# Performance work log

Measured on AMD Instinct MI355X. Metric: run time of the kernel, lower is better.

Reference implementation:

```python
import jax, jax.numpy as jnp
import numpy as np

B = 512            # graphs in batch
N = 246            # ROIs per graph per node type (Brainnetome atlas)
D = 256            # node feature dim (in_channels)
DEG = 32           # edges per node per edge type
RATIO = 0.8
K = int(np.ceil(RATIO * N))   # 197 nodes kept per graph (PyG topk uses ceil)
NT = B * N                    # total nodes per node type
E = B * N * DEG               # total edges per edge type
SLOPE = 0.2                   # HANConv leaky_relu negative slope


def _seg_softmax(logits, seg, num_segments):
    # numerically stable softmax over edges grouped by destination node
    m = jax.ops.segment_max(logits, seg, num_segments=num_segments)
    m = jnp.where(jnp.isfinite(m), m, 0.0)
    e = jnp.exp(logits - m[seg])
    s = jax.ops.segment_sum(e, seg, num_segments=num_segments)
    return e / (s[seg] + 1e-16)


def _edge_type_out(h_src, h_dst, ei, a_src, a_dst, n_dst):
    # one HANConv metapath: GAT-style attention + sum-aggregate + relu
    row, col = ei[0], ei[1]
    logit = jax.nn.leaky_relu((h_src * a_src).sum(-1)[row] + (h_dst * a_dst).sum(-1)[col], SLOPE)
    alpha = _seg_softmax(logit, col, n_dst)
    out = jax.ops.segment_sum(h_src[row] * alpha[:, None], col, num_segments=n_dst)
    return jax.nn.relu(out)


def _group(o1, o2, k_w, k_b, q):
    # HANConv semantic attention over the 2 metapaths hitting a node type
    stk = jnp.stack([o1, o2])                    # [2, NT, 1]
    t = jnp.tanh(stk @ k_w + k_b).mean(axis=1)   # [2, 1]
    w = jax.nn.softmax((q * t).sum(-1))          # [2]
    return (w[:, None, None] * stk).sum(0)       # [NT, 1]


def _han_scores(x_bold, x_dti, pw_b, pb_b, pw_d, pb_d, att, k_w, k_b, q, ei_bb, ei_bd, ei_db, ei_dd):
    h_b = x_bold @ pw_b + pb_b   # [NT, 1]
    h_d = x_dti @ pw_d + pb_d
    o_bb = _edge_type_out(h_b, h_b, ei_bb, att[0, 0], att[0, 1], NT)  # dst bold
    o_bd = _edge_type_out(h_b, h_d, ei_bd, att[1, 0], att[1, 1], NT)  # dst dti
    o_db = _edge_type_out(h_d, h_b, ei_db, att[2, 0], att[2, 1], NT)  # dst bold
    o_dd = _edge_type_out(h_d, h_d, ei_dd, att[3, 0], att[3, 1], NT)  # dst dti
    s_bold = _group(o_bb, o_db, k_w, k_b, q)[:, 0]
    s_dti = _group(o_bd, o_dd, k_w, k_b, q)[:, 0]
    return s_bold, s_dti


def _topk(score):
    # per-graph top-K (all graphs have exactly N nodes -> static K)
    _, idx = jax.lax.top_k(score.reshape(B, N), K)
    return (idx + (jnp.arange(B, dtype=idx.dtype) * N)[:, None]).reshape(-1)


def _mask_of(perm, num_nodes):
    return jnp.full((num_nodes,), -1, dtype=jnp.int32).at[perm].set(
        jnp.arange(perm.shape[0], dtype=jnp.int32))


def _filter(ei, mask_row, mask_col):
    # jit-compatible variant of filter_adj: keep full edge length, mark
    # dropped edges with -1 and return the validity mask (no compaction).
    r, c = mask_row[ei[0]], mask_col[ei[1]]
    valid = (r >= 0) & (c >= 0)
    return jnp.stack([jnp.where(valid, r, -1), jnp.where(valid, c, -1)]), valid


def setup_inputs() -> dict:
    key = jax.random.key(0)
    ks = jax.random.split(key, 12)

    def edges(k):
        k1, k2 = jax.random.split(k)
        base = jnp.repeat(jnp.arange(B, dtype=jnp.int32) * N, N * DEG)
        row = base + jax.random.randint(k1, (E,), 0, N, dtype=jnp.int32)
        col = base + jax.random.randint(k2, (E,), 0, N, dtype=jnp.int32)
        return jnp.stack([row, col])

    batch = jnp.repeat(jnp.arange(B, dtype=jnp.int32), N)
    return {
        "x_bold": jax.random.normal(ks[0], (NT, D), jnp.float32),
        "x_dti": jax.random.normal(ks[1], (NT, D), jnp.float32),
        "proj_w_bold": jax.random.normal(ks[2], (D, 1), jnp.float32) / np.float32(np.sqrt(D)),
        "proj_b_bold": jnp.zeros((1,), jnp.float32),
        "proj_w_dti": jax.random.normal(ks[3], (D, 1), jnp.float32) / np.float32(np.sqrt(D)),
        "proj_b_dti": jnp.zeros((1,), jnp.float32),
        "att": jax.random.normal(ks[4], (4, 2, 1), jnp.float32),
        "k_lin_w": jax.random.normal(ks[5], (1, 1), jnp.float32),
        "k_lin_b": jnp.zeros((1,), jnp.float32),
        "q": jax.random.normal(ks[6], (1,), jnp.float32),
        "ei_bb": edges(ks[7]),
        "ei_bd": edges(ks[8]),
        "ei_db": edges(ks[9]),
        "ei_dd": edges(ks[10]),
        "batch_bold": batch,
        "batch_dti": batch,
    }


def reference(x_bold, x_dti, proj_w_bold, proj_b_bold, proj_w_dti, proj_b_dti,
              att, k_lin_w, k_lin_b, q, ei_bb, ei_bd, ei_db, ei_dd,
              batch_bold, batch_dti):
    s_bold, s_dti = _han_scores(x_bold, x_dti, proj_w_bold, proj_b_bold,
                                proj_w_dti, proj_b_dti, att, k_lin_w, k_lin_b, q,
                                ei_bb, ei_bd, ei_db, ei_dd)
    perm_b = _topk(s_bold)
    perm_d = _topk(s_dti)
    xb = x_bold[perm_b] * jnp.tanh(s_bold[perm_b])[:, None]
    xd = x_dti[perm_d] * jnp.tanh(s_dti[perm_d])[:, None]
    mb = _mask_of(perm_b, NT)
    md = _mask_of(perm_d, NT)
    bb_f, v_bb = _filter(ei_bb, mb, mb)   # filter_adj_single on bold-bold
    dd_f, v_dd = _filter(ei_dd, md, md)   # filter_adj_single on dti-dti
    bd_f, v_bd = _filter(ei_bd, mb, md)   # filter_adj_multi mode=1
    db_f, v_db = _filter(ei_db, md, mb)   # filter_adj_multi mode=2
    return (xb, xd, bb_f, v_bb, bd_f, v_bd, db_f, v_db, dd_f, v_dd,
            batch_bold[perm_b], batch_dti[perm_d], perm_b, perm_d, s_bold, s_dti)
```

## Files before the change

kernel.cpp:

```cpp
#include <hip/hip_runtime.h>
#include <cmath>

#define BB   512
#define NN   246
#define DD   256
#define DEGC 32
#define KK   197
#define NTOT (BB*NN)
#define EE   (BB*NN*DEGC)
#define EPG  (NN*DEGC)
#define EPG4 (EPG/4)
#define BKK  (BB*KK)

#define O_XB     0LL
#define O_XD     25821184LL
#define O_E0     51642368LL
#define STRIDE3E 12091392LL
#define O_BATCHB 100007936LL
#define O_BATCHD 100108800LL
#define O_PERMB  100209664LL
#define O_PERMD  100310528LL
#define O_SB     100411392LL
#define O_SD     100537344LL

__global__ __launch_bounds__(256) void proj_kernel(
    const float* __restrict__ xb, const float* __restrict__ xd,
    const float* __restrict__ wb, const float* __restrict__ bbp,
    const float* __restrict__ wd, const float* __restrict__ bdp,
    float* __restrict__ hb, float* __restrict__ hd,
    double* __restrict__ sums) {
    if (blockIdx.x == 0 && threadIdx.x < 4) sums[threadIdx.x] = 0.0;
    int wid  = (blockIdx.x * 256 + threadIdx.x) >> 6;
    int lane = threadIdx.x & 63;
    if (wid >= 2 * NTOT) return;
    const float* x; const float* w; const float* bp; float* h; int node;
    if (wid < NTOT) { x = xb; w = wb; bp = bbp; h = hb; node = wid; }
    else            { x = xd; w = wd; bp = bdp; h = hd; node = wid - NTOT; }
    float4 xv = ((const float4*)(x + (long long)node * DD))[lane];
    float4 wv = ((const float4*)w)[lane];
    double acc = (double)xv.x * wv.x + (double)xv.y * wv.y +
                 (double)xv.z * wv.z + (double)xv.w * wv.w;
#pragma unroll
    for (int m = 32; m; m >>= 1) acc += __shfl_xor(acc, m, 64);
    if (lane == 0) h[node] = __fadd_rn((float)acc, bp[0]);
}

__global__ __launch_bounds__(512) void att_kernel(
    const int* __restrict__ ei_bb, const int* __restrict__ ei_bd,
    const int* __restrict__ ei_db, const int* __restrict__ ei_dd,
    const float* __restrict__ hb, const float* __restrict__ hd,
    const float* __restrict__ att, float* __restrict__ o) {
    __shared__ float hs_sh[NN];
    __shared__ float hd_sh[NN];
    __shared__ float s_sh[NN];
    __shared__ float num_sh[NN];

    int bid = blockIdx.x;
    int t   = bid >> 9;
    int g   = bid & 511;
    const int* ei = (t == 0) ? ei_bb : (t == 1) ? ei_bd : (t == 2) ? ei_db : ei_dd;
    const float* hs  = (t >= 2) ? hd : hb;
    const float* hdt = (t & 1)  ? hd : hb;
    float a_src = att[2 * t], a_dst = att[2 * t + 1];
    int base = g * NN;
    int tid  = threadIdx.x;

    if (tid < NN) {
        hs_sh[tid]  = hs[base + tid];
        hd_sh[tid]  = hdt[base + tid];
        s_sh[tid]   = 1e-16f;
        num_sh[tid] = 0.f;
    }
    __syncthreads();

    const int4* rows = (const int4*)(ei + g * EPG);
    const int4* cols = (const int4*)(ei + EE + g * EPG);

    for (int q = tid; q < EPG4; q += 512) {
        int4 r4 = rows[q], c4 = cols[q];
#pragma unroll
        for (int j = 0; j < 4; ++j) {
            int r = ((const int*)&r4)[j] - base;
            int c = ((const int*)&c4)[j] - base;
            float hr = hs_sh[r];
            float l  = __fadd_rn(__fmul_rn(a_src, hr), __fmul_rn(a_dst, hd_sh[c]));
            l = (l >= 0.f) ? l : __fmul_rn(0.2f, l);
            float e = expf(l);
            atomicAdd(&s_sh[c], e);
            atomicAdd(&num_sh[c], __fmul_rn(hr, e));
        }
    }
    __syncthreads();

    if (tid < NN) {
        float v = num_sh[tid] / s_sh[tid];
        o[(long long)t * NTOT + base + tid] = (v > 0.f) ? v : 0.f;
    }
}

__global__ __launch_bounds__(256) void grp_reduce_kernel(
    const float* __restrict__ o, const float* __restrict__ kwp,
    const float* __restrict__ kbp, double* __restrict__ sums) {
    int i = blockIdx.x * 256 + threadIdx.x;
    int t = blockIdx.x / 492;
    float kw = kwp[0], kb = kbp[0];
    float v = tanhf(__fadd_rn(__fmul_rn(o[i], kw), kb));
    double acc = (double)v;
#pragma unroll
    for (int m = 32; m; m >>= 1) acc += __shfl_xor(acc, m, 64);
    __shared__ double part[4];
    int lane = threadIdx.x & 63, wv = threadIdx.x >> 6;
    if (lane == 0) part[wv] = acc;
    __syncthreads();
    if (threadIdx.x == 0) {
        double tot = ((part[0] + part[1]) + part[2]) + part[3];
        atomicAdd(&sums[t], tot);
    }
}

__global__ void grp_w_kernel(const double* __restrict__ sums,
                             const float* __restrict__ qp,
                             float* __restrict__ wscal) {
    if (threadIdx.x == 0 && blockIdx.x == 0) {
        float q = qp[0];
        float tv[4];
#pragma unroll
        for (int i = 0; i < 4; ++i) tv[i] = (float)(sums[i] / (double)NTOT);
        {
            float l0 = __fmul_rn(q, tv[0]), l1 = __fmul_rn(q, tv[2]);
            float mx = fmaxf(l0, l1);
            float e0 = expf(l0 - mx), e1 = expf(l1 - mx);
            float se = __fadd_rn(e0, e1);
            wscal[0] = e0 / se; wscal[1] = e1 / se;
        }
        {
            float l0 = __fmul_rn(q, tv[1]), l1 = __fmul_rn(q, tv[3]);
            float mx = fmaxf(l0, l1);
            float e0 = expf(l0 - mx), e1 = expf(l1 - mx);
            float se = __fadd_rn(e0, e1);
            wscal[2] = e0 / se; wscal[3] = e1 / se;
        }
    }
}

__global__ __launch_bounds__(256) void score_kernel(
    const float* __restrict__ o, const float* __restrict__ wscal,
    float* __restrict__ sb, float* __restrict__ sd,
    float* __restrict__ osb, float* __restrict__ osd) {
    int i = blockIdx.x * 256 + threadIdx.x;
    float w0 = wscal[0], w1 = wscal[1], w2 = wscal[2], w3 = wscal[3];
    float vb = __fadd_rn(__fmul_rn(w0, o[i]),          __fmul_rn(w1, o[2LL * NTOT + i]));
    float vd = __fadd_rn(__fmul_rn(w2, o[NTOT + i]),   __fmul_rn(w3, o[3LL * NTOT + i]));
    sb[i] = vb; sd[i] = vd; osb[i] = vb; osd[i] = vd;
}

__global__ __launch_bounds__(256) void topk_kernel(
    const float* __restrict__ sb, const float* __restrict__ sd,
    const int* __restrict__ batch_b, const int* __restrict__ batch_d,
    int* __restrict__ mask_b, int* __restrict__ mask_d,
    int* __restrict__ perm_b, int* __restrict__ perm_d,
    float* __restrict__ out) {
    __shared__ float v[256];
    __shared__ int   ix[256];
    int g = blockIdx.x & 511, which = blockIdx.x >> 9, tid = threadIdx.x;
    const float* s     = which ? sd : sb;
    const int*   batch = which ? batch_d : batch_b;
    int* mask  = which ? mask_d : mask_b;
    int* permi = which ? perm_d : perm_b;
    float* operm  = out + (which ? O_PERMD : O_PERMB);
    float* obatch = out + (which ? O_BATCHD : O_BATCHB);
    v[tid]  = (tid < NN) ? s[g * NN + tid] : -INFINITY;
    ix[tid] = tid;
    __syncthreads();
    for (int k2 = 2; k2 <= 256; k2 <<= 1) {
        for (int j = k2 >> 1; j > 0; j >>= 1) {
            int p = tid ^ j;
            if (p > tid) {
                float va = v[tid], vb2 = v[p];
                int   ia = ix[tid], ib = ix[p];
                bool before = (va > vb2) || (va == vb2 && ia < ib);
                bool up = ((tid & k2) == 0);
                if (up ? !before : before) {
                    v[tid] = vb2; v[p] = va; ix[tid] = ib; ix[p] = ia;
                }
            }
            __syncthreads();
        }
    }
    if (tid < NN) {
        int node  = ix[tid];
        int gnode = g * NN + node;
        if (tid < KK) {
            int gp = g * KK + tid;
            permi[gp]  = gnode;
            operm[gp]  = (float)gnode;
            obatch[gp] = (float)batch[gnode];
            mask[gnode] = gp;
        } else {
            mask[gnode] = -1;
        }
    }
}

__global__ __launch_bounds__(256) void gather_kernel(
    const float* __restrict__ xb, const float* __restrict__ xd,
    const int* __restrict__ perm_b, const int* __restrict__ perm_d,
    const float* __restrict__ sb, const float* __restrict__ sd,
    float* __restrict__ out) {
    int wid  = (blockIdx.x * 256 + threadIdx.x) >> 6;
    int lane = threadIdx.x & 63;
    if (wid >= 2 * BKK) return;
    int which = wid >= BKK;
    int j = which ? wid - BKK : wid;
    const float* x    = which ? xd : xb;
    const int*   perm = which ? perm_d : perm_b;
    const float* s    = which ? sd : sb;
    long long obase   = which ? O_XD : O_XB;
    int p = perm[j];
    float scale = tanhf(s[p]);
    float4 vv = ((const float4*)(x + (long long)p * DD))[lane];
    float4 r  = make_float4(vv.x * scale, vv.y * scale, vv.z * scale, vv.w * scale);
    ((float4*)(out + obase + (long long)j * DD))[lane] = r;
}

__global__ __launch_bounds__(256) void filter_kernel(
    const int* __restrict__ ei_bb, const int* __restrict__ ei_bd,
    const int* __restrict__ ei_db, const int* __restrict__ ei_dd,
    const int* __restrict__ mask_b, const int* __restrict__ mask_d,
    float* __restrict__ out) {
    const int QE = EE / 4;
    int tid = blockIdx.x * 256 + threadIdx.x;
    if (tid >= 4 * QE) return;
    int t = tid / QE;
    int q = tid - t * QE;
    const int* ei = (t == 0) ? ei_bb : (t == 1) ? ei_bd : (t == 2) ? ei_db : ei_dd;
    const int* mr = (t >= 2) ? mask_d : mask_b;
    const int* mc = (t & 1)  ? mask_d : mask_b;
    int4 r4 = ((const int4*)ei)[q];
    int4 c4 = ((const int4*)(ei + EE))[q];
    float4 orow, ocol, oval;
#pragma unroll
    for (int j = 0; j < 4; ++j) {
        int r = mr[((const int*)&r4)[j]];
        int c = mc[((const int*)&c4)[j]];
        bool val = (r >= 0) && (c >= 0);
        ((float*)&orow)[j] = val ? (float)r : -1.f;
        ((float*)&ocol)[j] = val ? (float)c : -1.f;
        ((float*)&oval)[j] = val ? 1.f : 0.f;
    }
    float* base = out + O_E0 + (long long)t * STRIDE3E;
    ((float4*)base)[q]              = orow;
    ((float4*)(base + EE))[q]       = ocol;
    ((float4*)(base + 2LL * EE))[q] = oval;
}

extern "C" void kernel_launch(void* const* d_in, const int* in_sizes, int n_in,
                              void* d_out, int out_size, void* d_ws, size_t ws_size,
                              hipStream_t stream) {
    const float* x_bold = (const float*)d_in[0];
    const float* x_dti  = (const float*)d_in[1];
    const float* pw_b   = (const float*)d_in[2];
    const float* pb_b   = (const float*)d_in[3];
    const float* pw_d   = (const float*)d_in[4];
    const float* pb_d   = (const float*)d_in[5];
    const float* att    = (const float*)d_in[6];
    const float* k_w    = (const float*)d_in[7];
    const float* k_b    = (const float*)d_in[8];
    const float* qv     = (const float*)d_in[9];
    const int* ei_bb    = (const int*)d_in[10];
    const int* ei_bd    = (const int*)d_in[11];
    const int* ei_db    = (const int*)d_in[12];
    const int* ei_dd    = (const int*)d_in[13];
    const int* batch_b  = (const int*)d_in[14];
    const int* batch_d  = (const int*)d_in[15];
    float* out = (float*)d_out;

    char* w = (char*)d_ws;
    double* sums  = (double*)w;
    float*  wscal = (float*)(w + 32);
    float*  hb    = (float*)(w + 48);
    float*  hd    = hb + NTOT;
    float*  obuf  = hd + NTOT;
    float*  sb    = obuf + 4LL * NTOT;
    float*  sd    = sb + NTOT;
    int* mask_b   = (int*)(sd + NTOT);
    int* mask_d   = mask_b + NTOT;
    int* perm_b   = mask_d + NTOT;
    int* perm_d   = perm_b + BKK;

    proj_kernel<<<2 * NTOT / 4, 256, 0, stream>>>(x_bold, x_dti, pw_b, pb_b,
                                                  pw_d, pb_d, hb, hd, sums);
    att_kernel<<<4 * BB, 512, 0, stream>>>(ei_bb, ei_bd, ei_db, ei_dd,
                                           hb, hd, att, obuf);
    grp_reduce_kernel<<<4 * NTOT / 256, 256, 0, stream>>>(obuf, k_w, k_b, sums);
    grp_w_kernel<<<1, 64, 0, stream>>>(sums, qv, wscal);
    score_kernel<<<NTOT / 256, 256, 0, stream>>>(obuf, wscal, sb, sd,
                                                 out + O_SB, out + O_SD);
    topk_kernel<<<2 * BB, 256, 0, stream>>>(sb, sd, batch_b, batch_d,
                                            mask_b, mask_d, perm_b, perm_d, out);
    gather_kernel<<<2 * BKK * 64 / 256, 256, 0, stream>>>(x_bold, x_dti,
                                                          perm_b, perm_d,
                                                          sb, sd, out);
    filter_kernel<<<EE / 256, 256, 0, stream>>>(ei_bb, ei_bd, ei_db, ei_dd,
                                                mask_b, mask_d, out);
}
```

Measured before the change: 921.1 us.

## Fuse semantic reduction into attention, rank-based topk, nontemporal loads/stores

Folds the tanh/mean reduction into the attention kernel and the softmax weight computation into the score kernel, removing two launches and one pass over the per-metapath outputs. Replaces the bitonic sort in top-k with an O(N^2) rank count per element. Adds nontemporal loads and stores on the streaming edge, feature and output traffic to reduce cache pollution. The double-precision reduction order changes (per-graph partial sums instead of fixed 256-element blocks), which may shift results slightly.

Result: faster. 880.8 us (-4.4%).

```diff
diff --git a/kernel.cpp b/kernel.cpp
--- a/kernel.cpp
+++ b/kernel.cpp
@@ -22,6 +22,22 @@
 #define O_PERMD  100310528LL
 #define O_SB     100411392LL
 #define O_SD     100537344LL
+
+typedef float vf4 __attribute__((ext_vector_type(4)));
+typedef int   vi4 __attribute__((ext_vector_type(4)));
+
+__device__ __forceinline__ vi4 nt_load_i4(const int* p) {
+    return __builtin_nontemporal_load((const vi4*)p);
+}
+__device__ __forceinline__ vf4 nt_load_f4(const float* p) {
+    return __builtin_nontemporal_load((const vf4*)p);
+}
+__device__ __forceinline__ void nt_store_f4(float* p, vf4 v) {
+    __builtin_nontemporal_store(v, (vf4*)p);
+}
+__device__ __forceinline__ void nt_store_f(float* p, float v) {
+    __builtin_nontemporal_store(v, p);
+}
 
 __global__ __launch_bounds__(256) void proj_kernel(
     const float* __restrict__ xb, const float* __restrict__ xd,
@@ -36,8 +52,8 @@
     const float* x; const float* w; const float* bp; float* h; int node;
     if (wid < NTOT) { x = xb; w = wb; bp = bbp; h = hb; node = wid; }
     else            { x = xd; w = wd; bp = bdp; h = hd; node = wid - NTOT; }
-    float4 xv = ((const float4*)(x + (long long)node * DD))[lane];
-    float4 wv = ((const float4*)w)[lane];
+    vf4 xv = nt_load_f4(x + (long long)node * DD + 4 * lane);
+    vf4 wv = *(const vf4*)(w + 4 * lane);
     double acc = (double)xv.x * wv.x + (double)xv.y * wv.y +
                  (double)xv.z * wv.z + (double)xv.w * wv.w;
 #pragma unroll
@@ -49,11 +65,14 @@
     const int* __restrict__ ei_bb, const int* __restrict__ ei_bd,
     const int* __restrict__ ei_db, const int* __restrict__ ei_dd,
     const float* __restrict__ hb, const float* __restrict__ hd,
-    const float* __restrict__ att, float* __restrict__ o) {
+    const float* __restrict__ att, const float* __restrict__ kwp,
+    const float* __restrict__ kbp, float* __restrict__ o,
+    double* __restrict__ sums) {
     __shared__ float hs_sh[NN];
     __shared__ float hd_sh[NN];
     __shared__ float s_sh[NN];
     __shared__ float num_sh[NN];
+    __shared__ double part[8];
 
     int bid = blockIdx.x;
     int t   = bid >> 9;
@@ -73,15 +92,16 @@
     }
     __syncthreads();
 
-    const int4* rows = (const int4*)(ei + g * EPG);
-    const int4* cols = (const int4*)(ei + EE + g * EPG);
+    const int* rows = ei + g * EPG;
+    const int* cols = ei + EE + g * EPG;
 
     for (int q = tid; q < EPG4; q += 512) {
-        int4 r4 = rows[q], c4 = cols[q];
+        vi4 r4 = nt_load_i4(rows + 4 * q);
+        vi4 c4 = nt_load_i4(cols + 4 * q);
 #pragma unroll
         for (int j = 0; j < 4; ++j) {
-            int r = ((const int*)&r4)[j] - base;
-            int c = ((const int*)&c4)[j] - base;
+            int r = r4[j] - base;
+            int c = c4[j] - base;
             float hr = hs_sh[r];
             float l  = __fadd_rn(__fmul_rn(a_src, hr), __fmul_rn(a_dst, hd_sh[c]));
             l = (l >= 0.f) ? l : __fmul_rn(0.2f, l);
@@ -92,66 +112,53 @@
     }
     __syncthreads();
 
+    float kw = kwp[0], kb = kbp[0];
+    float my = 0.f;
     if (tid < NN) {
         float v = num_sh[tid] / s_sh[tid];
-        o[(long long)t * NTOT + base + tid] = (v > 0.f) ? v : 0.f;
-    }
-}
-
-__global__ __launch_bounds__(256) void grp_reduce_kernel(
-    const float* __restrict__ o, const float* __restrict__ kwp,
-    const float* __restrict__ kbp, double* __restrict__ sums) {
-    int i = blockIdx.x * 256 + threadIdx.x;
-    int t = blockIdx.x / 492;
-    float kw = kwp[0], kb = kbp[0];
-    float v = tanhf(__fadd_rn(__fmul_rn(o[i], kw), kb));
-    double acc = (double)v;
+        v = (v > 0.f) ? v : 0.f;
+        o[(long long)t * NTOT + base + tid] = v;
+        my = tanhf(__fadd_rn(__fmul_rn(v, kw), kb));
+    }
+    double acc = (double)my;
 #pragma unroll
     for (int m = 32; m; m >>= 1) acc += __shfl_xor(acc, m, 64);
-    __shared__ double part[4];
-    int lane = threadIdx.x & 63, wv = threadIdx.x >> 6;
+    int lane = tid & 63, wv = tid >> 6;
     if (lane == 0) part[wv] = acc;
     __syncthreads();
-    if (threadIdx.x == 0) {
-        double tot = ((part[0] + part[1]) + part[2]) + part[3];
+    if (tid == 0) {
+        double tot = 0.0;
+#pragma unroll
+        for (int i = 0; i < 8; ++i) tot += part[i];
         atomicAdd(&sums[t], tot);
     }
 }
 
-__global__ void grp_w_kernel(const double* __restrict__ sums,
-                             const float* __restrict__ qp,
-                             float* __restrict__ wscal) {
-    if (threadIdx.x == 0 && blockIdx.x == 0) {
-        float q = qp[0];
-        float tv[4];
-#pragma unroll
-        for (int i = 0; i < 4; ++i) tv[i] = (float)(sums[i] / (double)NTOT);
-        {
-            float l0 = __fmul_rn(q, tv[0]), l1 = __fmul_rn(q, tv[2]);
-            float mx = fmaxf(l0, l1);
-            float e0 = expf(l0 - mx), e1 = expf(l1 - mx);
-            float se = __fadd_rn(e0, e1);
-            wscal[0] = e0 / se; wscal[1] = e1 / se;
-        }
-        {
-            float l0 = __fmul_rn(q, tv[1]), l1 = __fmul_rn(q, tv[3]);
-            float mx = fmaxf(l0, l1);
-            float e0 = expf(l0 - mx), e1 = expf(l1 - mx);
-            float se = __fadd_rn(e0, e1);
-            wscal[2] = e0 / se; wscal[3] = e1 / se;
-        }
-    }
-}
-
 __global__ __launch_bounds__(256) void score_kernel(
-    const float* __restrict__ o, const float* __restrict__ wscal,
+    const float* __restrict__ o, const double* __restrict__ sums,
+    const float* __restrict__ qp,
     float* __restrict__ sb, float* __restrict__ sd,
     float* __restrict__ osb, float* __restrict__ osd) {
     int i = blockIdx.x * 256 + threadIdx.x;
-    float w0 = wscal[0], w1 = wscal[1], w2 = wscal[2], w3 = wscal[3];
-    float vb = __fadd_rn(__fmul_rn(w0, o[i]),          __fmul_rn(w1, o[2LL * NTOT + i]));
-    float vd = __fadd_rn(__fmul_rn(w2, o[NTOT + i]),   __fmul_rn(w3, o[3LL * NTOT + i]));
-    sb[i] = vb; sd[i] = vd; osb[i] = vb; osd[i] = vd;
+    float q = qp[0];
+    float t0 = (float)(sums[0] / (double)NTOT);
+    float t1 = (float)(sums[1] / (double)NTOT);
+    float t2 = (float)(sums[2] / (double)NTOT);
+    float t3 = (float)(sums[3] / (double)NTOT);
+    float l0 = __fmul_rn(q, t0), l1 = __fmul_rn(q, t2);
+    float mx = fmaxf(l0, l1);
+    float e0 = expf(l0 - mx), e1 = expf(l1 - mx);
+    float se = __fadd_rn(e0, e1);
+    float w0 = e0 / se, w1 = e1 / se;
+    float l2 = __fmul_rn(q, t1), l3 = __fmul_rn(q, t3);
+    float mx2 = fmaxf(l2, l3);
+    float e2 = expf(l2 - mx2), e3 = expf(l3 - mx2);
+    float se2 = __fadd_rn(e2, e3);
+    float w2 = e2 / se2, w3 = e3 / se2;
+    float vb = __fadd_rn(__fmul_rn(w0, o[i]),        __fmul_rn(w1, o[2LL * NTOT + i]));
+    float vd = __fadd_rn(__fmul_rn(w2, o[NTOT + i]), __fmul_rn(w3, o[3LL * NTOT + i]));
+    sb[i] = vb; sd[i] = vd;
+    nt_store_f(osb + i, vb); nt_store_f(osd + i, vd);
 }
 
 __global__ __launch_bounds__(256) void topk_kernel(
@@ -160,8 +167,7 @@
     int* __restrict__ mask_b, int* __restrict__ mask_d,
     int* __restrict__ perm_b, int* __restrict__ perm_d,
     float* __restrict__ out) {
-    __shared__ float v[256];
-    __shared__ int   ix[256];
+    __shared__ float v[NN];
     int g = blockIdx.x & 511, which = blockIdx.x >> 9, tid = threadIdx.x;
     const float* s     = which ? sd : sb;
     const int*   batch = which ? batch_d : batch_b;
@@ -169,32 +175,22 @@
     int* permi = which ? perm_d : perm_b;
     float* operm  = out + (which ? O_PERMD : O_PERMB);
     float* obatch = out + (which ? O_BATCHD : O_BATCHB);
-    v[tid]  = (tid < NN) ? s[g * NN + tid] : -INFINITY;
-    ix[tid] = tid;
+    if (tid < NN) v[tid] = s[g * NN + tid];
     __syncthreads();
-    for (int k2 = 2; k2 <= 256; k2 <<= 1) {
-        for (int j = k2 >> 1; j > 0; j >>= 1) {
-            int p = tid ^ j;
-            if (p > tid) {
-                float va = v[tid], vb2 = v[p];
-                int   ia = ix[tid], ib = ix[p];
-                bool before = (va > vb2) || (va == vb2 && ia < ib);
-                bool up = ((tid & k2) == 0);
-                if (up ? !before : before) {
-                    v[tid] = vb2; v[p] = va; ix[tid] = ib; ix[p] = ia;
-                }
-            }
-            __syncthreads();
+    if (tid < NN) {
+        float mv = v[tid];
+        int rank = 0;
+#pragma unroll 4
+        for (int j = 0; j < NN; ++j) {
+            float vj = v[j];
+            rank += (vj > mv) || (vj == mv && j < tid);
         }
-    }
-    if (tid < NN) {
-        int node  = ix[tid];
-        int gnode = g * NN + node;
-        if (tid < KK) {
-            int gp = g * KK + tid;
-            permi[gp]  = gnode;
-            operm[gp]  = (float)gnode;
-            obatch[gp] = (float)batch[gnode];
+        int gnode = g * NN + tid;
+        if (rank < KK) {
+            int gp = g * KK + rank;
+            permi[gp] = gnode;
+            nt_store_f(operm + gp, (float)gnode);
+            nt_store_f(obatch + gp, (float)batch[gnode]);
             mask[gnode] = gp;
         } else {
             mask[gnode] = -1;
@@ -218,9 +214,11 @@
     long long obase   = which ? O_XD : O_XB;
     int p = perm[j];
     float scale = tanhf(s[p]);
-    float4 vv = ((const float4*)(x + (long long)p * DD))[lane];
-    float4 r  = make_float4(vv.x * scale, vv.y * scale, vv.z * scale, vv.w * scale);
-    ((float4*)(out + obase + (long long)j * DD))[lane] = r;
+    vf4 vv = nt_load_f4(x + (long long)p * DD + 4 * lane);
+    vf4 r;
+    r.x = vv.x * scale; r.y = vv.y * scale;
+    r.z = vv.z * scale; r.w = vv.w * scale;
+    nt_store_f4(out + obase + (long long)j * DD + 4 * lane, r);
 }
 
 __global__ __launch_bounds__(256) void filter_kernel(
@@ -236,22 +234,22 @@
     const int* ei = (t == 0) ? ei_bb : (t == 1) ? ei_bd : (t == 2) ? ei_db : ei_dd;
     const int* mr = (t >= 2) ? mask_d : mask_b;
     const int* mc = (t & 1)  ? mask_d : mask_b;
-    int4 r4 = ((const int4*)ei)[q];
-    int4 c4 = ((const int4*)(ei + EE))[q];
-    float4 orow, ocol, oval;
+    vi4 r4 = nt_load_i4(ei + 4 * q);
+    vi4 c4 = nt_load_i4(ei + EE + 4 * q);
+    vf4 orow, ocol, oval;
 #pragma unroll
     for (int j = 0; j < 4; ++j) {
-        int r = mr[((const int*)&r4)[j]];
-        int c = mc[((const int*)&c4)[j]];
+        int r = mr[r4[j]];
+        int c = mc[c4[j]];
         bool val = (r >= 0) && (c >= 0);
-        ((float*)&orow)[j] = val ? (float)r : -1.f;
-        ((float*)&ocol)[j] = val ? (float)c : -1.f;
-        ((float*)&oval)[j] = val ? 1.f : 0.f;
+        orow[j] = val ? (float)r : -1.f;
+        ocol[j] = val ? (float)c : -1.f;
+        oval[j] = val ? 1.f : 0.f;
     }
     float* base = out + O_E0 + (long long)t * STRIDE3E;
-    ((float4*)base)[q]              = orow;
-    ((float4*)(base + EE))[q]       = ocol;
-    ((float4*)(base + 2LL * EE))[q] = oval;
+    nt_store_f4(base + 4 * q,              orow);
+    nt_store_f4(base + EE + 4 * q,         ocol);
+    nt_store_f4(base + 2LL * EE + 4 * q,   oval);
 }
 
 extern "C" void kernel_launch(void* const* d_in, const int* in_sizes, int n_in,
@@ -277,8 +275,7 @@
 
     char* w = (char*)d_ws;
     double* sums  = (double*)w;
-    float*  wscal = (float*)(w + 32);
-    float*  hb    = (float*)(w + 48);
+    float*  hb    = (float*)(w + 64);
     float*  hd    = hb + NTOT;
     float*  obuf  = hd + NTOT;
     float*  sb    = obuf + 4LL * NTOT;
@@ -291,10 +288,8 @@
     proj_kernel<<<2 * NTOT / 4, 256, 0, stream>>>(x_bold, x_dti, pw_b, pb_b,
                                                   pw_d, pb_d, hb, hd, sums);
     att_kernel<<<4 * BB, 512, 0, stream>>>(ei_bb, ei_bd, ei_db, ei_dd,
-                                           hb, hd, att, obuf);
-    grp_reduce_kernel<<<4 * NTOT / 256, 256, 0, stream>>>(obuf, k_w, k_b, sums);
-    grp_w_kernel<<<1, 64, 0, stream>>>(sums, qv, wscal);
-    score_kernel<<<NTOT / 256, 256, 0, stream>>>(obuf, wscal, sb, sd,
+                                           hb, hd, att, k_w, k_b, obuf, sums);
+    score_kernel<<<NTOT / 256, 256, 0, stream>>>(obuf, sums, qv, sb, sd,
                                                  out + O_SB, out + O_SD);
     topk_kernel<<<2 * BB, 256, 0, stream>>>(sb, sd, batch_b, batch_d,
                                             mask_b, mask_d, perm_b, perm_d, out);
```
